# Kernel tuning notes

Measured on AMD Instinct MI355X. Metric: run time of the kernel, lower is better.

The kernel has to match this reference:

```python
import jax, jax.numpy as jnp
import numpy as np

N, IN, OUT, E, S = 65536, 512, 512, 8, 64


def setup_inputs() -> dict:
    key = jax.random.key(0)
    k1, k2, k3, k4, k5 = jax.random.split(key, 5)
    bound = float(np.sqrt(1.0 / IN))
    x = jax.random.normal(k1, (N, IN), dtype=jnp.float32)
    expert_coefficients = jax.random.normal(k2, (S, E), dtype=jnp.float32)
    batch_indices = jax.random.randint(k3, (N,), 0, S)
    weights = jax.random.uniform(k4, (E, OUT, IN), dtype=jnp.float32, minval=-bound, maxval=bound)
    bias = jax.random.uniform(k5, (OUT,), dtype=jnp.float32, minval=-bound, maxval=bound)
    return {"x": x, "expert_coefficients": expert_coefficients,
            "batch_indices": batch_indices, "weights": weights, "bias": bias}


def reference(x, expert_coefficients, batch_indices, weights, bias):
    # Original computes mixed_weights[b] = sum_e coeff[b,e] * W[e], then for each
    # system b applies mixed_weights[b] to the atoms with batch_indices == b via a
    # masked scan. Linearity lets us equivalently gather per-atom expert
    # coefficients and contract once, avoiding the O(num_systems * N) waste:
    #   out[n,o] = sum_e coeff[batch_indices[n], e] * sum_i W[e,o,i] * x[n,i]
    coeff_per_atom = expert_coefficients[batch_indices]  # [N, E]
    out = jnp.einsum('ni,eoi,ne->no', x, weights, coeff_per_atom)  # [N, OUT]
    return out + bias
```

## Files before the change

kernel.cpp:

```cpp
#include <hip/hip_runtime.h>
#include <hip/hip_bf16.h>

#define NA   65536
#define DIN  512
#define DOUT 512
#define NE   8
#define NS   64
#define CAP  1280
#define BM   128
#define BN   128
#define BK   32
#define TPS  (CAP / BM)
#define NKT  (DIN / BK)
#define CSTR 32

typedef __attribute__((ext_vector_type(8))) __bf16 bf16x8;
typedef __attribute__((ext_vector_type(4))) float floatx4;

__device__ __forceinline__ void async_load16(const void* g, void* l) {
  __builtin_amdgcn_global_load_lds(
      (__attribute__((address_space(1))) void*)(void*)g,
      (__attribute__((address_space(3))) void*)l,
      16, 0, 0);
}

__global__ void scatter_kernel(const int* __restrict__ bidx,
                               int* __restrict__ counts,
                               int* __restrict__ perm) {
  __shared__ int hist[NS];
  __shared__ int base[NS];
  int t = threadIdx.x;
  if (t < NS) hist[t] = 0;
  __syncthreads();
  int n = blockIdx.x * 256 + t;
  int s = bidx[n];
  int rank = atomicAdd(&hist[s], 1);
  __syncthreads();
  if (t < NS && hist[t] > 0) base[t] = atomicAdd(&counts[t * CSTR], hist[t]);
  __syncthreads();
  perm[s * CAP + base[s] + rank] = n;
}

__global__ void mixw_kernel(const float* __restrict__ W,
                            const float* __restrict__ coeff,
                            ushort* __restrict__ mixedW) {
  int t = threadIdx.x;
  int base = blockIdx.x * 2048 + t * 8;
  float w[NE][8];
#pragma unroll
  for (int e = 0; e < NE; e++) {
    const float4* p = (const float4*)(W + e * (DOUT * DIN) + base);
    float4 a = p[0], b = p[1];
    w[e][0] = a.x; w[e][1] = a.y; w[e][2] = a.z; w[e][3] = a.w;
    w[e][4] = b.x; w[e][5] = b.y; w[e][6] = b.z; w[e][7] = b.w;
  }
  int s0 = blockIdx.y * 8;
  for (int si = 0; si < 8; si++) {
    int s = s0 + si;
    float o[8] = {0, 0, 0, 0, 0, 0, 0, 0};
#pragma unroll
    for (int e = 0; e < NE; e++) {
      float c = coeff[s * NE + e];
#pragma unroll
      for (int j = 0; j < 8; j++) o[j] += c * w[e][j];
    }
    union { bf16x8 v; uint4 u; } cv;
#pragma unroll
    for (int j = 0; j < 8; j++) cv.v[j] = (__bf16)o[j];
    *(uint4*)(mixedW + (size_t)s * (DOUT * DIN) + base) = cv.u;
  }
}

__global__ __launch_bounds__(256) void gemm_kernel(
    const float* __restrict__ x, const ushort* __restrict__ mixedW,
    const int* __restrict__ perm, const int* __restrict__ counts,
    const float* __restrict__ bias, float* __restrict__ out) {
  int nwg = gridDim.x * gridDim.y;
  int lin = blockIdx.y * gridDim.x + blockIdx.x;
  int cpx = nwg >> 3;
  int work = (lin & 7) * cpx + (lin >> 3);
  int bx = work & 3;
  int by = work >> 2;

  int s = by / TPS;
  int tt = by - s * TPS;
  int count = counts[s * CSTR];
  int r0 = tt * BM;
  if (r0 >= count) return;
  int rows = min(BM, count - r0);
  int n0 = bx * BN;

  __shared__ __align__(16) float  Alds[3][BM * BK];
  __shared__ __align__(16) ushort Blds[3][BN * BK];
  __shared__ int prow[BM];

  int tid = threadIdx.x;
  int lane = tid & 63;
  int wave = tid >> 6;

  if (tid < BM) prow[tid] = perm[s * CAP + r0 + min(tid, rows - 1)];

  const float* aptr[4];
  int aoff[4];
#pragma unroll
  for (int j = 0; j < 4; j++) {
    int region = j * 4 + wave;
    int arow = region * 8 + (lane >> 3);
    int pr = perm[s * CAP + r0 + min(arow, rows - 1)];
    aptr[j] = x + (size_t)pr * DIN + (lane & 7) * 4;
    aoff[j] = region * 256;
  }
  const ushort* bptr[2];
  int boff[2];
#pragma unroll
  for (int j = 0; j < 2; j++) {
    int region = j * 4 + wave;
    int brow = region * 16 + (lane >> 2);
    bptr[j] = mixedW + (size_t)s * (DOUT * DIN) + (size_t)(n0 + brow) * DIN +
              (lane & 3) * 8;
    boff[j] = region * 512;
  }

  floatx4 acc[4][4];
#pragma unroll
  for (int mt = 0; mt < 4; mt++)
#pragma unroll
    for (int nt = 0; nt < 4; nt++) acc[mt][nt] = {0.f, 0.f, 0.f, 0.f};

  int wm = wave >> 1, wn = wave & 1;
  int m15 = lane & 15, quad = lane >> 4;

  __syncthreads();

#pragma unroll
  for (int t0 = 0; t0 < 2; t0++) {
#pragma unroll
    for (int j = 0; j < 4; j++)
      async_load16(aptr[j] + t0 * BK, Alds[t0] + aoff[j]);
#pragma unroll
    for (int j = 0; j < 2; j++)
      async_load16(bptr[j] + t0 * BK, Blds[t0] + boff[j]);
  }

  for (int t = 0; t < NKT; ++t) {
    if (t + 2 < NKT) {
      int nb = (t + 2) % 3;
#pragma unroll
      for (int j = 0; j < 4; j++)
        async_load16(aptr[j] + (t + 2) * BK, Alds[nb] + aoff[j]);
#pragma unroll
      for (int j = 0; j < 2; j++)
        async_load16(bptr[j] + (t + 2) * BK, Blds[nb] + boff[j]);
      asm volatile("s_waitcnt vmcnt(12)" ::: "memory");
    } else if (t == NKT - 2) {
      asm volatile("s_waitcnt vmcnt(6)" ::: "memory");
    } else {
      asm volatile("s_waitcnt vmcnt(0)" ::: "memory");
    }
    __builtin_amdgcn_s_barrier();
    __builtin_amdgcn_sched_barrier(0);

    int cb = t % 3;
    bf16x8 af[4], bfm[4];
#pragma unroll
    for (int i = 0; i < 4; i++) {
      const float* ap = Alds[cb] + (wm * 64 + i * 16 + m15) * BK + quad * 8;
      floatx4 lo = *(const floatx4*)ap;
      floatx4 hi = *(const floatx4*)(ap + 4);
#pragma unroll
      for (int k = 0; k < 4; k++) {
        af[i][k] = (__bf16)lo[k];
        af[i][4 + k] = (__bf16)hi[k];
      }
      bfm[i] = *(const bf16x8*)(Blds[cb] + (wn * 64 + i * 16 + m15) * BK + quad * 8);
    }
#pragma unroll
    for (int mt = 0; mt < 4; mt++)
#pragma unroll
      for (int nt = 0; nt < 4; nt++)
        acc[mt][nt] = __builtin_amdgcn_mfma_f32_16x16x32_bf16(
            af[mt], bfm[nt], acc[mt][nt], 0, 0, 0);

    __builtin_amdgcn_sched_barrier(0);
    __builtin_amdgcn_s_barrier();
  }

  float bv[4];
#pragma unroll
  for (int nt = 0; nt < 4; nt++) bv[nt] = bias[n0 + wn * 64 + nt * 16 + m15];

#pragma unroll
  for (int mt = 0; mt < 4; mt++) {
    int rb = wm * 64 + mt * 16 + quad * 4;
    int pr[4];
#pragma unroll
    for (int r = 0; r < 4; r++) pr[r] = prow[rb + r];
#pragma unroll
    for (int nt = 0; nt < 4; nt++) {
      int col = n0 + wn * 64 + nt * 16 + m15;
#pragma unroll
      for (int r = 0; r < 4; r++) {
        if (rb + r < rows)
          out[(size_t)pr[r] * DOUT + col] = acc[mt][nt][r] + bv[nt];
      }
    }
  }
}

extern "C" void kernel_launch(void* const* d_in, const int* in_sizes, int n_in,
                              void* d_out, int out_size, void* d_ws,
                              size_t ws_size, hipStream_t stream) {
  const float* x     = (const float*)d_in[0];
  const float* coeff = (const float*)d_in[1];
  const int*   bidx  = (const int*)d_in[2];
  const float* W     = (const float*)d_in[3];
  const float* bias  = (const float*)d_in[4];
  float* out = (float*)d_out;

  char* ws = (char*)d_ws;
  int* counts    = (int*)ws;
  int* perm      = (int*)(ws + NS * CSTR * 4);
  ushort* mixedW = (ushort*)(ws + NS * CSTR * 4 + NS * CAP * 4);

  hipMemsetAsync(counts, 0, NS * CSTR * sizeof(int), stream);
  hipLaunchKernelGGL(scatter_kernel, dim3(NA / 256), dim3(256), 0, stream,
                     bidx, counts, perm);
  hipLaunchKernelGGL(mixw_kernel, dim3(DOUT * DIN / 2048, 8), dim3(256), 0,
                     stream, W, coeff, mixedW);
  hipLaunchKernelGGL(gemm_kernel, dim3(DOUT / BN, NS * TPS), dim3(256), 0,
                     stream, x, mixedW, perm, counts, bias, out);
}
```

Measured before the change: 358.0 us.

## Convert A tile to bf16 in registers before LDS, with XOR-swizzled layout

The A operand (fp32 activations) is now loaded through registers and converted to bf16 before being written to LDS, instead of being copied to LDS as fp32 via async loads and converted on every fragment read. This halves the A footprint in LDS and the LDS read traffic. An XOR swizzle is applied to the A and B LDS layouts to reduce bank conflicts. The pipeline is restructured with a register double buffer, so the global load for tile t+2 overlaps the conversion write for tile t+1. The trade-off is more VGPR pressure and a synchronous global-load path for A in place of direct-to-LDS copies.

```diff
diff --git a/kernel.cpp b/kernel.cpp
--- a/kernel.cpp
+++ b/kernel.cpp
@@ -13,6 +13,7 @@
 #define TPS  (CAP / BM)
 #define NKT  (DIN / BK)
 #define CSTR 32
+#define TILE_US 4096
 
 typedef __attribute__((ext_vector_type(8))) __bf16 bf16x8;
 typedef __attribute__((ext_vector_type(4))) float floatx4;
@@ -23,6 +24,8 @@
       (__attribute__((address_space(3))) void*)l,
       16, 0, 0);
 }
+
+__device__ __forceinline__ int b3(int c) { return c >= 3 ? c - 3 : c; }
 
 __global__ void scatter_kernel(const int* __restrict__ bidx,
                                int* __restrict__ counts,
@@ -71,6 +74,30 @@
   }
 }
 
+__device__ __forceinline__ void gload_a(const float* g0, const float* g1,
+                                        int kt, float4& s0, float4& s1,
+                                        float4& s2, float4& s3) {
+  const float* a0 = g0 + kt * BK;
+  const float* a1 = g1 + kt * BK;
+  s0 = *(const float4*)(a0);
+  s1 = *(const float4*)(a0 + 4);
+  s2 = *(const float4*)(a1);
+  s3 = *(const float4*)(a1 + 4);
+}
+
+__device__ __forceinline__ void cvt_write(ushort* Ab, int wo0, int wo1,
+                                          const float4& s0, const float4& s1,
+                                          const float4& s2, const float4& s3) {
+  bf16x8 h;
+  h[0] = (__bf16)s0.x; h[1] = (__bf16)s0.y; h[2] = (__bf16)s0.z; h[3] = (__bf16)s0.w;
+  h[4] = (__bf16)s1.x; h[5] = (__bf16)s1.y; h[6] = (__bf16)s1.z; h[7] = (__bf16)s1.w;
+  *(bf16x8*)(Ab + wo0) = h;
+  bf16x8 g;
+  g[0] = (__bf16)s2.x; g[1] = (__bf16)s2.y; g[2] = (__bf16)s2.z; g[3] = (__bf16)s2.w;
+  g[4] = (__bf16)s3.x; g[5] = (__bf16)s3.y; g[6] = (__bf16)s3.z; g[7] = (__bf16)s3.w;
+  *(bf16x8*)(Ab + wo1) = g;
+}
+
 __global__ __launch_bounds__(256) void gemm_kernel(
     const float* __restrict__ x, const ushort* __restrict__ mixedW,
     const int* __restrict__ perm, const int* __restrict__ counts,
@@ -90,8 +117,8 @@
   int rows = min(BM, count - r0);
   int n0 = bx * BN;
 
-  __shared__ __align__(16) float  Alds[3][BM * BK];
-  __shared__ __align__(16) ushort Blds[3][BN * BK];
+  __shared__ __align__(16) ushort Alds[3 * TILE_US];
+  __shared__ __align__(16) ushort Blds[3 * TILE_US];
   __shared__ int prow[BM];
 
   int tid = threadIdx.x;
@@ -100,25 +127,33 @@
 
   if (tid < BM) prow[tid] = perm[s * CAP + r0 + min(tid, rows - 1)];
 
-  const float* aptr[4];
-  int aoff[4];
-#pragma unroll
-  for (int j = 0; j < 4; j++) {
-    int region = j * 4 + wave;
-    int arow = region * 8 + (lane >> 3);
-    int pr = perm[s * CAP + r0 + min(arow, rows - 1)];
-    aptr[j] = x + (size_t)pr * DIN + (lane & 7) * 4;
-    aoff[j] = region * 256;
-  }
-  const ushort* bptr[2];
-  int boff[2];
-#pragma unroll
-  for (int j = 0; j < 2; j++) {
-    int region = j * 4 + wave;
-    int brow = region * 16 + (lane >> 2);
-    bptr[j] = mixedW + (size_t)s * (DOUT * DIN) + (size_t)(n0 + brow) * DIN +
-              (lane & 3) * 8;
-    boff[j] = region * 512;
+  int chunk = lane & 3;
+  int cxor = (lane >> 3) & 3;
+  const float* agp0;
+  const float* agp1;
+  int awoff0, awoff1;
+  {
+    int rl0 = wave * 32 + (lane >> 2);
+    int rl1 = rl0 + 16;
+    int pr0 = perm[s * CAP + r0 + min(rl0, rows - 1)];
+    int pr1 = perm[s * CAP + r0 + min(rl1, rows - 1)];
+    agp0 = x + (size_t)pr0 * DIN + chunk * 8;
+    agp1 = x + (size_t)pr1 * DIN + chunk * 8;
+    int ac = chunk ^ cxor;
+    awoff0 = rl0 * 32 + ac * 8;
+    awoff1 = rl1 * 32 + ac * 8;
+  }
+  const ushort* bgp0;
+  const ushort* bgp1;
+  int boff0, boff1;
+  {
+    int bkc = (chunk ^ cxor) * 8;
+    int row0 = (wave * 16) + (lane >> 2);
+    int row1 = row0 + 64;
+    bgp0 = mixedW + (size_t)s * (DOUT * DIN) + (size_t)(n0 + row0) * DIN + bkc;
+    bgp1 = mixedW + (size_t)s * (DOUT * DIN) + (size_t)(n0 + row1) * DIN + bkc;
+    boff0 = wave * 512;
+    boff1 = (4 + wave) * 512;
   }
 
   floatx4 acc[4][4];
@@ -129,61 +164,68 @@
 
   int wm = wave >> 1, wn = wave & 1;
   int m15 = lane & 15, quad = lane >> 4;
-
-  __syncthreads();
-
-#pragma unroll
-  for (int t0 = 0; t0 < 2; t0++) {
-#pragma unroll
-    for (int j = 0; j < 4; j++)
-      async_load16(aptr[j] + t0 * BK, Alds[t0] + aoff[j]);
-#pragma unroll
-    for (int j = 0; j < 2; j++)
-      async_load16(bptr[j] + t0 * BK, Blds[t0] + boff[j]);
-  }
-
-  for (int t = 0; t < NKT; ++t) {
-    if (t + 2 < NKT) {
-      int nb = (t + 2) % 3;
-#pragma unroll
-      for (int j = 0; j < 4; j++)
-        async_load16(aptr[j] + (t + 2) * BK, Alds[nb] + aoff[j]);
-#pragma unroll
-      for (int j = 0; j < 2; j++)
-        async_load16(bptr[j] + (t + 2) * BK, Blds[nb] + boff[j]);
-      asm volatile("s_waitcnt vmcnt(12)" ::: "memory");
-    } else if (t == NKT - 2) {
-      asm volatile("s_waitcnt vmcnt(6)" ::: "memory");
-    } else {
-      asm volatile("s_waitcnt vmcnt(0)" ::: "memory");
-    }
-    __builtin_amdgcn_s_barrier();
-    __builtin_amdgcn_sched_barrier(0);
-
-    int cb = t % 3;
-    bf16x8 af[4], bfm[4];
-#pragma unroll
-    for (int i = 0; i < 4; i++) {
-      const float* ap = Alds[cb] + (wm * 64 + i * 16 + m15) * BK + quad * 8;
-      floatx4 lo = *(const floatx4*)ap;
-      floatx4 hi = *(const floatx4*)(ap + 4);
-#pragma unroll
-      for (int k = 0; k < 4; k++) {
-        af[i][k] = (__bf16)lo[k];
-        af[i][4 + k] = (__bf16)hi[k];
-      }
-      bfm[i] = *(const bf16x8*)(Blds[cb] + (wn * 64 + i * 16 + m15) * BK + quad * 8);
-    }
-#pragma unroll
-    for (int mt = 0; mt < 4; mt++)
-#pragma unroll
-      for (int nt = 0; nt < 4; nt++)
-        acc[mt][nt] = __builtin_amdgcn_mfma_f32_16x16x32_bf16(
-            af[mt], bfm[nt], acc[mt][nt], 0, 0, 0);
-
-    __builtin_amdgcn_sched_barrier(0);
-    __builtin_amdgcn_s_barrier();
-  }
+  int rxor = (m15 >> 1) & 3;
+  int rcol = (quad ^ rxor) * 8;
+  int aro = (wm * 64 + m15) * 32 + rcol;
+  int bro = (wn * 64 + m15) * 32 + rcol;
+
+  float4 p0, p1, p2, p3, q0, q1, q2, q3;
+
+  gload_a(agp0, agp1, 0, p0, p1, p2, p3);
+  async_load16(bgp0, Blds + boff0);
+  async_load16(bgp1, Blds + boff1);
+  gload_a(agp0, agp1, 1, q0, q1, q2, q3);
+  async_load16(bgp0 + BK, Blds + TILE_US + boff0);
+  async_load16(bgp1 + BK, Blds + TILE_US + boff1);
+  asm volatile("s_waitcnt vmcnt(8)" ::: "memory");
+  cvt_write(Alds, awoff0, awoff1, p0, p1, p2, p3);
+
+#define ITER(T, C0, C1, C2, C3, N0, N1, N2, N3)                        \
+  {                                                                    \
+    if ((T) + 2 < NKT) {                                               \
+      int c2 = b3(c0 + 2);                                             \
+      gload_a(agp0, agp1, (T) + 2, N0, N1, N2, N3);                    \
+      async_load16(bgp0 + ((T) + 2) * BK, Blds + c2 * TILE_US + boff0);\
+      async_load16(bgp1 + ((T) + 2) * BK, Blds + c2 * TILE_US + boff1);\
+      asm volatile("s_waitcnt vmcnt(8)" ::: "memory");                 \
+    } else if ((T) == NKT - 2) {                                       \
+      asm volatile("s_waitcnt vmcnt(2)" ::: "memory");                 \
+    } else {                                                           \
+      asm volatile("s_waitcnt vmcnt(0)" ::: "memory");                 \
+    }                                                                  \
+    __builtin_amdgcn_s_barrier();                                      \
+    __builtin_amdgcn_sched_barrier(0);                                 \
+    if ((T) + 1 < NKT)                                                 \
+      cvt_write(Alds + b3(c0 + 1) * TILE_US, awoff0, awoff1,           \
+                C0, C1, C2, C3);                                       \
+    {                                                                  \
+      const ushort* Ab = Alds + c0 * TILE_US;                          \
+      const ushort* Bb = Blds + c0 * TILE_US;                          \
+      bf16x8 af[4], bfm[4];                                            \
+      _Pragma("unroll")                                                \
+      for (int i = 0; i < 4; i++) {                                    \
+        af[i]  = *(const bf16x8*)(Ab + aro + i * 512);                 \
+        bfm[i] = *(const bf16x8*)(Bb + bro + i * 512);                 \
+      }                                                                \
+      _Pragma("unroll")                                                \
+      for (int mt = 0; mt < 4; mt++)                                   \
+        _Pragma("unroll")                                              \
+        for (int nt = 0; nt < 4; nt++)                                 \
+          acc[mt][nt] = __builtin_amdgcn_mfma_f32_16x16x32_bf16(       \
+              af[mt], bfm[nt], acc[mt][nt], 0, 0, 0);                  \
+    }                                                                  \
+    asm volatile("s_waitcnt lgkmcnt(0)" ::: "memory");                 \
+    __builtin_amdgcn_sched_barrier(0);                                 \
+    __builtin_amdgcn_s_barrier();                                      \
+    c0 = b3(c0 + 1);                                                   \
+  }
+
+  int c0 = 0;
+  for (int t = 0; t < NKT; t += 2) {
+    ITER(t,     q0, q1, q2, q3, p0, p1, p2, p3);
+    ITER(t + 1, p0, p1, p2, p3, q0, q1, q2, q3);
+  }
+#undef ITER
 
   float bv[4];
 #pragma unroll
```

Measured after the change: 343.4 us. 1.04x faster.
